# Performance work log

Measured on AMD Instinct MI355X. Metric: run time of the kernel, lower is better.

The kernel has to match this reference:

```python
import jax, jax.numpy as jnp
import numpy as np

B = 512          # batch
IN_UNITS = 8     # primary capsule dim
IN_CH = 1152     # number of primary capsules
NUM_UNITS = 10   # output capsules (classes)
UNIT_SIZE = 16   # output capsule dim
BETA = 1.45      # squash beta: 1.45 - 0.22*(ep_iter/total) with ep_iter = n_iter = 0
NUM_ROUTING = 3


def setup_inputs() -> dict:
    key = jax.random.key(0)
    k1, k2 = jax.random.split(key)
    x = jax.random.normal(k1, (B, IN_UNITS, IN_CH), dtype=jnp.float32)
    # W parameter: torch shape (1, in_channels, num_units, unit_size, in_units); drop leading 1
    W = jax.random.normal(k2, (IN_CH, NUM_UNITS, UNIT_SIZE, IN_UNITS), dtype=jnp.float32)
    return {"x": x, "W": W}


def _squash(s):
    # s: (B, num_units, unit_size). Torch squash sums dim=2 of (B,1,nu,us,1),
    # which is the num_units axis (axis=1 here). Faithful to source.
    mag_sq = jnp.sum(s * s, axis=1, keepdims=True)          # (B,1,us)
    mag = jnp.sqrt(mag_sq)
    return mag_sq / (BETA + mag_sq) * (s / mag)


def reference(x, W):
    # u_hat[b,i,j,u] = sum_k W[i,j,u,k] * x[b,k,i]
    u_hat = jnp.einsum('ijuk,bki->biju', W, x)               # (B, IN_CH, NUM_UNITS, UNIT_SIZE)
    b_ij = jnp.zeros((IN_CH, NUM_UNITS), dtype=x.dtype)
    v = None
    for _ in range(NUM_ROUTING):
        c = jax.nn.softmax(b_ij, axis=0)                     # softmax over in_channels (dim=1 in torch)
        s = jnp.einsum('ij,biju->bju', c, u_hat)             # (B, NUM_UNITS, UNIT_SIZE)
        v = _squash(s)
        # b update: agreement <u_hat, v>, averaged over batch
        b_ij = jnp.einsum('biju,bju->ij', u_hat, v) / u_hat.shape[0]
    # rearrange 'b c (g h) w -> b c g (h w)' with g=4, w=1 -> reshape (B, nu, 4, us//4)
    return v.reshape(v.shape[0], NUM_UNITS, 4, UNIT_SIZE // 4)
```

## Files before the change

### kernel.cpp

```cpp
#include <hip/hip_runtime.h>
#include <hip/hip_bf16.h>
#include <math.h>

#define B    512
#define INU  8
#define IC   1152
#define NU   10
#define US   16
#define JU   160
#define KI   9216
#define BETAC 1.45f
#define NSPLIT 32
#define KC 288

typedef __attribute__((ext_vector_type(8))) __bf16 bf16x8;
typedef __attribute__((ext_vector_type(4))) float floatx4;

static __device__ __forceinline__ unsigned short f2bf(float f) {
  unsigned u = __builtin_bit_cast(unsigned, f);
  u = (u + 0x7fffu + ((u >> 16) & 1u)) >> 16;
  return (unsigned short)u;
}
static __device__ __forceinline__ float bf2f(unsigned short h) {
  return __builtin_bit_cast(float, ((unsigned)h) << 16);
}
static __device__ __forceinline__ uint4 scale8(uint4 wv, float4 cA, float4 cB) {
  union { uint4 u; unsigned short s[8]; } in;
  in.u = wv;
  union { uint4 u; __hip_bfloat162 h[4]; } o;
  o.h[0] = __float22bfloat162_rn(make_float2(bf2f(in.s[0]) * cA.x, bf2f(in.s[1]) * cA.y));
  o.h[1] = __float22bfloat162_rn(make_float2(bf2f(in.s[2]) * cA.z, bf2f(in.s[3]) * cA.w));
  o.h[2] = __float22bfloat162_rn(make_float2(bf2f(in.s[4]) * cB.x, bf2f(in.s[5]) * cB.y));
  o.h[3] = __float22bfloat162_rn(make_float2(bf2f(in.s[6]) * cB.z, bf2f(in.s[7]) * cB.w));
  return o.u;
}

__global__ __launch_bounds__(256) void prep_kernel(
    const float* __restrict__ x, const float* __restrict__ W,
    unsigned short* __restrict__ xb, unsigned short* __restrict__ xT,
    unsigned short* __restrict__ Wt, float* __restrict__ cT) {
  __shared__ float ts[64 * 65];
  int id = blockIdx.x;
  int t = threadIdx.x;
  if (id < 1152) {
    int k0 = (id % 144) * 64;
    int b0 = (id / 144) * 64;
#pragma unroll
    for (int r = 0; r < 16; ++r) {
      int idx = t + 256 * r;
      int br = idx >> 6, kc = idx & 63;
      float v = x[(size_t)(b0 + br) * KI + k0 + kc];
      ts[br * 65 + kc] = v;
      xb[(size_t)(b0 + br) * KI + k0 + kc] = f2bf(v);
    }
    __syncthreads();
#pragma unroll
    for (int r = 0; r < 8; ++r) {
      int idx = t + 256 * r;
      int kr = idx >> 5, bc = (idx & 31) * 2;
      unsigned lo = f2bf(ts[bc * 65 + kr]);
      unsigned hi = f2bf(ts[(bc + 1) * 65 + kr]);
      *(unsigned*)&xT[(size_t)(k0 + kr) * B + b0 + bc] = lo | (hi << 16);
    }
  } else {
    int e = (id - 1152) * 256 + t;
    int ju = e / KI;
    int rem = e - ju * KI;
    int k = rem / IC;
    int i = rem - k * IC;
    Wt[e] = f2bf(W[(size_t)i * 1280 + ju * 8 + k]);
    if (id == 1152) {
      for (int q = t; q < IC * NU; q += 256) cT[q] = 1.0f / (float)IC;
    }
  }
}

__global__ __launch_bounds__(256) void s_gemm_mfma(
    const unsigned short* __restrict__ xb, const unsigned short* __restrict__ Wt,
    const float* __restrict__ cT, float* __restrict__ sp) {
  int b0 = blockIdx.x * 64;
  int kbase = blockIdx.y * KC;
  int i0 = kbase % IC;
  int t = threadIdx.x;
  int w = t >> 6, lane = t & 63, col = lane & 15, quad = lane >> 4;
  __shared__ unsigned short xs[64 * 40];
  __shared__ unsigned short ms[160 * 40];
  __shared__ float cs[NU * KC];

  int xrow = t >> 2, xc = (t & 3) * 8;
  int mrow0 = t >> 2, mrow1 = (t + 256) >> 2, mrow2 = (t + 512) >> 2;
  int mc = (t & 3) * 8;
  int j0 = mrow0 >> 4, j1 = mrow1 >> 4, j2 = mrow2 >> 4;

  for (int ch = t; ch < NU * KC; ch += 256) {
    int j = ch / KC;
    cs[ch] = cT[j * IC + i0 + (ch - j * KC)];
  }

  uint4 xv, m0, m1, m2;
  auto prefetch = [&](int k0) {
    xv = *(const uint4*)&xb[(size_t)(b0 + xrow) * KI + k0 + xc];
    m0 = *(const uint4*)&Wt[(size_t)mrow0 * KI + k0 + mc];
    m1 = *(const uint4*)&Wt[(size_t)mrow1 * KI + k0 + mc];
    if (t < 128) m2 = *(const uint4*)&Wt[(size_t)mrow2 * KI + k0 + mc];
  };
  auto commit = [&](int off) {
    *(uint4*)&xs[xrow * 40 + xc] = xv;
    float4 a0 = *(const float4*)&cs[j0 * KC + off + mc];
    float4 a1 = *(const float4*)&cs[j0 * KC + off + mc + 4];
    *(uint4*)&ms[mrow0 * 40 + mc] = scale8(m0, a0, a1);
    float4 b0c = *(const float4*)&cs[j1 * KC + off + mc];
    float4 b1c = *(const float4*)&cs[j1 * KC + off + mc + 4];
    *(uint4*)&ms[mrow1 * 40 + mc] = scale8(m1, b0c, b1c);
    if (t < 128) {
      float4 d0 = *(const float4*)&cs[j2 * KC + off + mc];
      float4 d1 = *(const float4*)&cs[j2 * KC + off + mc + 4];
      *(uint4*)&ms[mrow2 * 40 + mc] = scale8(m2, d0, d1);
    }
  };

  floatx4 acc[10];
#pragma unroll
  for (int jt = 0; jt < 10; ++jt) acc[jt] = (floatx4){0.f, 0.f, 0.f, 0.f};

  prefetch(kbase);
  __syncthreads();
  const int nsteps = KC >> 5;
  for (int s = 0; s < nsteps; ++s) {
    commit(s * 32);
    __syncthreads();
    if (s + 1 < nsteps) prefetch(kbase + (s + 1) * 32);
    bf16x8 a = *(bf16x8*)&xs[(w * 16 + col) * 40 + quad * 8];
#pragma unroll
    for (int jt = 0; jt < 10; ++jt) {
      bf16x8 bb = *(bf16x8*)&ms[(jt * 16 + col) * 40 + quad * 8];
      acc[jt] = __builtin_amdgcn_mfma_f32_16x16x32_bf16(a, bb, acc[jt], 0, 0, 0);
    }
    __syncthreads();
  }
#pragma unroll
  for (int jt = 0; jt < 10; ++jt)
#pragma unroll
    for (int r = 0; r < 4; ++r) {
      int b = b0 + w * 16 + quad * 4 + r;
      sp[((size_t)blockIdx.y * B + b) * JU + jt * 16 + col] = acc[jt][r];
    }
}

__global__ __launch_bounds__(192) void squash_kernel(
    const float* __restrict__ sp, unsigned short* __restrict__ vT,
    float* __restrict__ out) {
  int b = blockIdx.x;
  int t = threadIdx.x;
  __shared__ float sv[JU];
  __shared__ float fac[US];
  float s = 0.0f;
  if (t < JU) {
#pragma unroll
    for (int k = 0; k < NSPLIT; ++k) s += sp[((size_t)k * B + b) * JU + t];
    sv[t] = s;
  }
  __syncthreads();
  if (t < US) {
    float m = 0.0f;
#pragma unroll
    for (int j = 0; j < NU; ++j) {
      float q = sv[j * US + t];
      m += q * q;
    }
    fac[t] = sqrtf(m) / (BETAC + m);
  }
  __syncthreads();
  if (t < JU) {
    float val = s * fac[t & 15];
    vT[(size_t)t * B + b] = f2bf(val);
    if (out) out[(size_t)b * JU + t] = val;
  }
}

__global__ __launch_bounds__(256) void b_update_mfma(
    const unsigned short* __restrict__ xT, const unsigned short* __restrict__ vT,
    const float* __restrict__ W, float* __restrict__ bp) {
  int k = blockIdx.x / 18;
  int i0 = (blockIdx.x - k * 18) * 64;
  int bs = blockIdx.y;
  size_t ki0 = (size_t)k * IC + i0;
  int t = threadIdx.x;
  int w = t >> 6, lane = t & 63, col = lane & 15, quad = lane >> 4;
  __shared__ unsigned short xs[64 * 40];
  __shared__ unsigned short vs[160 * 40];

  int xrow = t >> 2, xc = (t & 3) * 8;
  int mrow0 = t >> 2, mrow1 = (t + 256) >> 2, mrow2 = (t + 512) >> 2;
  int mc = (t & 3) * 8;
  uint4 xv, m0, m1, m2;

  auto prefetch = [&](int c0) {
    xv = *(const uint4*)&xT[(ki0 + xrow) * B + c0 + xc];
    m0 = *(const uint4*)&vT[(size_t)mrow0 * B + c0 + mc];
    m1 = *(const uint4*)&vT[(size_t)mrow1 * B + c0 + mc];
    if (t < 128) m2 = *(const uint4*)&vT[(size_t)mrow2 * B + c0 + mc];
  };
  auto commit = [&]() {
    *(uint4*)&xs[xrow * 40 + xc] = xv;
    *(uint4*)&vs[mrow0 * 40 + mc] = m0;
    *(uint4*)&vs[mrow1 * 40 + mc] = m1;
    if (t < 128) *(uint4*)&vs[mrow2 * 40 + mc] = m2;
  };

  floatx4 acc[10];
#pragma unroll
  for (int jt = 0; jt < 10; ++jt) acc[jt] = (floatx4){0.f, 0.f, 0.f, 0.f};

  prefetch(bs * 256);
  for (int s = 0; s < 8; ++s) {
    commit();
    __syncthreads();
    if (s < 7) prefetch(bs * 256 + (s + 1) * 32);
    bf16x8 a = *(bf16x8*)&xs[(w * 16 + col) * 40 + quad * 8];
#pragma unroll
    for (int jt = 0; jt < 10; ++jt) {
      bf16x8 bb = *(bf16x8*)&vs[(jt * 16 + col) * 40 + quad * 8];
      acc[jt] = __builtin_amdgcn_mfma_f32_16x16x32_bf16(a, bb, acc[jt], 0, 0, 0);
    }
    __syncthreads();
  }
  int p = k * 2 + bs;
#pragma unroll
  for (int jt = 0; jt < 10; ++jt) {
#pragma unroll
    for (int r = 0; r < 4; ++r) {
      int i = i0 + w * 16 + quad * 4 + r;
      float wv = W[(size_t)i * 1280 + jt * 128 + col * 8 + k];
      float pr = wv * acc[jt][r];
      pr += __shfl_xor(pr, 1);
      pr += __shfl_xor(pr, 2);
      pr += __shfl_xor(pr, 4);
      pr += __shfl_xor(pr, 8);
      if (col == 0)
        bp[(size_t)p * (IC * NU) + jt * IC + i] = pr * (1.0f / (float)B);
    }
  }
}

__global__ __launch_bounds__(256) void softmax_c_kernel(
    const float* __restrict__ bp, float* __restrict__ cT) {
  int j = blockIdx.x;
  int t = threadIdx.x;
  __shared__ float bsum[IC];
  __shared__ float red[256];
  for (int i = t; i < IC; i += 256) {
    float s = 0.0f;
#pragma unroll
    for (int p = 0; p < 16; ++p) s += bp[(size_t)p * (IC * NU) + j * IC + i];
    bsum[i] = s;
  }
  __syncthreads();
  float m = -1e30f;
  for (int i = t; i < IC; i += 256) m = fmaxf(m, bsum[i]);
  red[t] = m;
  __syncthreads();
  for (int o = 128; o > 0; o >>= 1) {
    if (t < o) red[t] = fmaxf(red[t], red[t + o]);
    __syncthreads();
  }
  float mx = red[0];
  __syncthreads();
  float sm = 0.0f;
  for (int i = t; i < IC; i += 256) {
    float e = __expf(bsum[i] - mx);
    bsum[i] = e;
    sm += e;
  }
  red[t] = sm;
  __syncthreads();
  for (int o = 128; o > 0; o >>= 1) {
    if (t < o) red[t] += red[t + o];
    __syncthreads();
  }
  float inv = 1.0f / red[0];
  for (int i = t; i < IC; i += 256) cT[(size_t)j * IC + i] = bsum[i] * inv;
}

extern "C" void kernel_launch(void* const* d_in, const int* in_sizes, int n_in,
                              void* d_out, int out_size, void* d_ws,
                              size_t ws_size, hipStream_t stream) {
  const float* x = (const float*)d_in[0];
  const float* W = (const float*)d_in[1];
  float* out = (float*)d_out;

  char* pws = (char*)d_ws;
  float* cT = (float*)pws;                     pws += (size_t)NU * IC * 4;
  float* bp = (float*)pws;                     pws += (size_t)16 * IC * NU * 4;
  float* sp = (float*)pws;                     pws += (size_t)NSPLIT * B * JU * 4;
  unsigned short* xb = (unsigned short*)pws;   pws += (size_t)B * KI * 2;
  unsigned short* xT = (unsigned short*)pws;   pws += (size_t)KI * B * 2;
  unsigned short* Wt = (unsigned short*)pws;   pws += (size_t)JU * KI * 2;
  unsigned short* vT = (unsigned short*)pws;

  prep_kernel<<<1152 + 5760, 256, 0, stream>>>(x, W, xb, xT, Wt, cT);

  for (int it = 0; it < 3; ++it) {
    s_gemm_mfma<<<dim3(8, NSPLIT), 256, 0, stream>>>(xb, Wt, cT, sp);
    squash_kernel<<<B, 192, 0, stream>>>(sp, vT, (it == 2) ? out : nullptr);
    if (it < 2) {
      b_update_mfma<<<dim3(144, 2), 256, 0, stream>>>(xT, vT, W, bp);
      softmax_c_kernel<<<NU, 256, 0, stream>>>(bp, cT);
    }
  }
}
```

Before: 187.8 us.

## Tile W transpose through shared memory and add reordered fp32 W copy

The W-to-bf16 transpose in the prep kernel now runs through a shared-memory tile, 144 blocks of 32 channels by 320 columns, instead of one strided gather per element. That cuts uncoalesced reads and shrinks the grid. The prep kernel also writes an fp32 copy Wr laid out as [k][i][ju], so the epilogue of b_update reads W contiguously across lanes rather than with a stride of 8. The cost is an extra fp32 workspace buffer of 9216x160 and a larger shared tile in the prep kernel.

```diff
diff --git a/kernel.cpp b/kernel.cpp
--- a/kernel.cpp
+++ b/kernel.cpp
@@ -38,8 +38,9 @@
 __global__ __launch_bounds__(256) void prep_kernel(
     const float* __restrict__ x, const float* __restrict__ W,
     unsigned short* __restrict__ xb, unsigned short* __restrict__ xT,
-    unsigned short* __restrict__ Wt, float* __restrict__ cT) {
-  __shared__ float ts[64 * 65];
+    unsigned short* __restrict__ Wt, float* __restrict__ Wr,
+    float* __restrict__ cT) {
+  __shared__ float ts[32 * 322];
   int id = blockIdx.x;
   int t = threadIdx.x;
   if (id < 1152) {
@@ -63,12 +64,34 @@
       *(unsigned*)&xT[(size_t)(k0 + kr) * B + b0 + bc] = lo | (hi << 16);
     }
   } else {
-    int e = (id - 1152) * 256 + t;
-    int ju = e / KI;
-    int rem = e - ju * KI;
-    int k = rem / IC;
-    int i = rem - k * IC;
-    Wt[e] = f2bf(W[(size_t)i * 1280 + ju * 8 + k]);
+    int wid = id - 1152;
+    int i0 = (wid >> 2) * 32;
+    int c0 = (wid & 3) * 320;
+#pragma unroll
+    for (int r = 0; r < 20; ++r) {
+      int q = t + 256 * r;
+      int il = q / 160, c = (q - il * 160) * 2;
+      *(float2*)&ts[il * 322 + c] =
+          *(const float2*)&W[(size_t)(i0 + il) * 1280 + c0 + c];
+    }
+    __syncthreads();
+    {
+      int il2 = (t & 15) * 2;
+      for (int p = (t >> 4); p < 320; p += 16) {
+        int c = c0 + p;
+        int ju = c >> 3, k = c & 7;
+        unsigned lo = f2bf(ts[il2 * 322 + p]);
+        unsigned hi = f2bf(ts[(il2 + 1) * 322 + p]);
+        *(unsigned*)&Wt[(size_t)ju * KI + k * IC + i0 + il2] = lo | (hi << 16);
+      }
+    }
+    int ju0 = c0 >> 3;
+    for (int q = t; q < 8 * 32 * 40; q += 256) {
+      int k = q / 1280;
+      int il = (q / 40) & 31;
+      int jl = q - (q / 40) * 40;
+      Wr[((size_t)k * IC + i0 + il) * JU + ju0 + jl] = ts[il * 322 + jl * 8 + k];
+    }
     if (id == 1152) {
       for (int q = t; q < IC * NU; q += 256) cT[q] = 1.0f / (float)IC;
     }
@@ -96,7 +119,6 @@
     int j = ch / KC;
     cs[ch] = cT[j * IC + i0 + (ch - j * KC)];
   }
-
   uint4 xv, m0, m1, m2;
   auto prefetch = [&](int k0) {
     xv = *(const uint4*)&xb[(size_t)(b0 + xrow) * KI + k0 + xc];
@@ -118,11 +140,9 @@
       *(uint4*)&ms[mrow2 * 40 + mc] = scale8(m2, d0, d1);
     }
   };
-
   floatx4 acc[10];
 #pragma unroll
   for (int jt = 0; jt < 10; ++jt) acc[jt] = (floatx4){0.f, 0.f, 0.f, 0.f};
-
   prefetch(kbase);
   __syncthreads();
   const int nsteps = KC >> 5;
@@ -180,7 +200,7 @@
 
 __global__ __launch_bounds__(256) void b_update_mfma(
     const unsigned short* __restrict__ xT, const unsigned short* __restrict__ vT,
-    const float* __restrict__ W, float* __restrict__ bp) {
+    const float* __restrict__ Wr, float* __restrict__ bp) {
   int k = blockIdx.x / 18;
   int i0 = (blockIdx.x - k * 18) * 64;
   int bs = blockIdx.y;
@@ -189,12 +209,10 @@
   int w = t >> 6, lane = t & 63, col = lane & 15, quad = lane >> 4;
   __shared__ unsigned short xs[64 * 40];
   __shared__ unsigned short vs[160 * 40];
-
   int xrow = t >> 2, xc = (t & 3) * 8;
   int mrow0 = t >> 2, mrow1 = (t + 256) >> 2, mrow2 = (t + 512) >> 2;
   int mc = (t & 3) * 8;
   uint4 xv, m0, m1, m2;
-
   auto prefetch = [&](int c0) {
     xv = *(const uint4*)&xT[(ki0 + xrow) * B + c0 + xc];
     m0 = *(const uint4*)&vT[(size_t)mrow0 * B + c0 + mc];
@@ -207,11 +225,9 @@
     *(uint4*)&vs[mrow1 * 40 + mc] = m1;
     if (t < 128) *(uint4*)&vs[mrow2 * 40 + mc] = m2;
   };
-
   floatx4 acc[10];
 #pragma unroll
   for (int jt = 0; jt < 10; ++jt) acc[jt] = (floatx4){0.f, 0.f, 0.f, 0.f};
-
   prefetch(bs * 256);
   for (int s = 0; s < 8; ++s) {
     commit();
@@ -231,7 +247,7 @@
 #pragma unroll
     for (int r = 0; r < 4; ++r) {
       int i = i0 + w * 16 + quad * 4 + r;
-      float wv = W[(size_t)i * 1280 + jt * 128 + col * 8 + k];
+      float wv = Wr[((size_t)k * IC + i) * JU + jt * 16 + col];
       float pr = wv * acc[jt][r];
       pr += __shfl_xor(pr, 1);
       pr += __shfl_xor(pr, 2);
@@ -293,18 +309,19 @@
   float* cT = (float*)pws;                     pws += (size_t)NU * IC * 4;
   float* bp = (float*)pws;                     pws += (size_t)16 * IC * NU * 4;
   float* sp = (float*)pws;                     pws += (size_t)NSPLIT * B * JU * 4;
+  float* Wr = (float*)pws;                     pws += (size_t)KI * JU * 4;
   unsigned short* xb = (unsigned short*)pws;   pws += (size_t)B * KI * 2;
   unsigned short* xT = (unsigned short*)pws;   pws += (size_t)KI * B * 2;
   unsigned short* Wt = (unsigned short*)pws;   pws += (size_t)JU * KI * 2;
   unsigned short* vT = (unsigned short*)pws;
 
-  prep_kernel<<<1152 + 5760, 256, 0, stream>>>(x, W, xb, xT, Wt, cT);
+  prep_kernel<<<1152 + 144, 256, 0, stream>>>(x, W, xb, xT, Wt, Wr, cT);
 
   for (int it = 0; it < 3; ++it) {
     s_gemm_mfma<<<dim3(8, NSPLIT), 256, 0, stream>>>(xb, Wt, cT, sp);
     squash_kernel<<<B, 192, 0, stream>>>(sp, vT, (it == 2) ? out : nullptr);
     if (it < 2) {
-      b_update_mfma<<<dim3(144, 2), 256, 0, stream>>>(xT, vT, W, bp);
+      b_update_mfma<<<dim3(144, 2), 256, 0, stream>>>(xT, vT, Wr, bp);
       softmax_c_kernel<<<NU, 256, 0, stream>>>(bp, cT);
     }
   }
```

After: 176.9 us, median of 2. 5.8% less time.
